# Performance work log

Hardware: AMD Instinct MI355X
Metric: run time of the kernel (lower is better)

## Reference

```python
import jax, jax.numpy as jnp
import numpy as np

N_QUBITS = 4
N_LAYERS = 2


def _ry(theta):
    # PennyLane RY(theta) = [[cos(t/2), -sin(t/2)], [sin(t/2), cos(t/2)]]
    c = jnp.cos(theta / 2)
    s = jnp.sin(theta / 2)
    return jnp.stack([jnp.stack([c, -s]), jnp.stack([s, c])]).astype(jnp.complex64)


def _rz(theta):
    # PennyLane RZ(theta) = diag(exp(-i t/2), exp(+i t/2))
    e = jnp.exp(-0.5j * theta.astype(jnp.complex64))
    return jnp.diag(jnp.stack([e, jnp.conj(e)]))


def _apply_1q(state, U, wire):
    # state: (2,)*N_QUBITS complex; contract U into axis `wire`
    state = jnp.tensordot(U, state, axes=((1,), (wire,)))
    return jnp.moveaxis(state, 0, wire)


def _cnot(state, ctrl, tgt):
    s = jnp.moveaxis(state, ctrl, 0)
    t2 = tgt - 1 if tgt > ctrl else tgt
    s1 = jnp.flip(s[1], axis=t2)  # X on target where control == 1
    return jnp.moveaxis(jnp.stack([s[0], s1]), 0, ctrl)


def _circuit(angles, weights):
    # angles: (N_QUBITS,), weights: (N_LAYERS, N_QUBITS, 2)
    state = jnp.zeros((2,) * N_QUBITS, jnp.complex64).at[(0,) * N_QUBITS].set(1.0)
    for i in range(N_QUBITS):
        state = _apply_1q(state, _ry(angles[i]), i)
    for l in range(N_LAYERS):
        for i in range(N_QUBITS):
            state = _apply_1q(state, _ry(weights[l, i, 0]), i)
            state = _apply_1q(state, _rz(weights[l, i, 1]), i)
        for i in range(N_QUBITS - 1):
            state = _cnot(state, i, i + 1)
        state = _cnot(state, N_QUBITS - 1, 0)
    probs = jnp.abs(state) ** 2
    p = probs.reshape(2, -1).sum(axis=1)  # marginal on wire 0
    return p[0] - p[1]  # <Z_0>


def setup_inputs() -> dict:
    key = jax.random.key(0)
    ks = jax.random.split(key, 6)
    B = 65536
    return {
        "x": jax.random.normal(ks[0], (B, 256), jnp.float32),
        "W1": jax.random.normal(ks[1], (64, 256), jnp.float32) * 0.0625,
        "b1": jax.random.normal(ks[2], (64,), jnp.float32) * 0.01,
        "W2": jax.random.normal(ks[3], (4, 64), jnp.float32) * 0.125,
        "b2": jax.random.normal(ks[4], (4,), jnp.float32) * 0.01,
        "q_weights": jax.random.normal(ks[5], (N_LAYERS, N_QUBITS, 2), jnp.float32) * 0.1,
    }


def reference(x, W1, b1, W2, b2, q_weights):
    h = jax.nn.relu(x @ W1.T + b1)          # [B, 64]
    angles = jnp.tanh(h @ W2.T + b2)         # [B, 4]
    z = jax.vmap(lambda a: _circuit(a, q_weights))(angles)  # [B]
    return z[:, None]                        # [B, 1]
```

## Files before the change

### kernel.cpp

```cpp
#include <hip/hip_runtime.h>
#include <math.h>

typedef _Float16 half8   __attribute__((ext_vector_type(8)));
typedef _Float16 half4v  __attribute__((ext_vector_type(4)));
typedef float    float4v __attribute__((ext_vector_type(4)));

#define BM    64
#define KDIM  256
#define HSW   65

__global__ void w1_cvt(const float* __restrict__ W1, _Float16* __restrict__ w1h)
{
    int i = (blockIdx.x * 256 + threadIdx.x) * 4;
    float4v v = *(const float4v*)(W1 + i);
    half4v h;
    h[0] = (_Float16)v[0]; h[1] = (_Float16)v[1];
    h[2] = (_Float16)v[2]; h[3] = (_Float16)v[3];
    *(half4v*)(w1h + i) = h;
}

__global__ __launch_bounds__(256, 4)
void qc_fused(const float* __restrict__ x,
              const _Float16* __restrict__ w1h,
              const float* __restrict__ b1,
              const float* __restrict__ W2,
              const float* __restrict__ b2,
              const float* __restrict__ qw,
              float* __restrict__ out)
{
    __shared__ float hs[BM * HSW];
    __shared__ float angs[BM * 4];
    __shared__ float trig[32];

    const int tid  = threadIdx.x;
    const int lane = tid & 63;
    const int wv   = tid >> 6;
    const int m    = lane & 15;
    const int q    = lane >> 4;
    const int row0 = blockIdx.x * BM;

    if (tid < 8) {
        int l = tid >> 2, i = tid & 3;
        float wy = qw[(l * 4 + i) * 2 + 0];
        float wz = qw[(l * 4 + i) * 2 + 1];
        float sy, cy, sz, cz;
        sincosf(0.5f * wy, &sy, &cy);
        sincosf(0.5f * wz, &sz, &cz);
        trig[(l * 4 + i) * 4 + 0] = cy;
        trig[(l * 4 + i) * 4 + 1] = sy;
        trig[(l * 4 + i) * 4 + 2] = cz;
        trig[(l * 4 + i) * 4 + 3] = sz;
    }

    const float* xrow = x + (size_t)(row0 + wv * 16 + m) * KDIM + q * 8;
    half8 afr[8];
    #pragma unroll
    for (int f = 0; f < 8; ++f) {
        float4v v0 = *(const float4v*)(xrow + f * 32);
        float4v v1 = *(const float4v*)(xrow + f * 32 + 4);
        afr[f][0] = (_Float16)v0[0]; afr[f][1] = (_Float16)v0[1];
        afr[f][2] = (_Float16)v0[2]; afr[f][3] = (_Float16)v0[3];
        afr[f][4] = (_Float16)v1[0]; afr[f][5] = (_Float16)v1[1];
        afr[f][6] = (_Float16)v1[2]; afr[f][7] = (_Float16)v1[3];
    }

    float b1v[4];
    #pragma unroll
    for (int b = 0; b < 4; ++b) b1v[b] = b1[16 * b + m];

    float4v acc[4] = {};
    #pragma unroll
    for (int f = 0; f < 8; ++f) {
        const int ko = f * 32 + q * 8;
        #pragma unroll
        for (int b = 0; b < 4; ++b) {
            half8 bf = *(const half8*)(w1h + (size_t)(16 * b + m) * KDIM + ko);
            acc[b] = __builtin_amdgcn_mfma_f32_16x16x32_f16(afr[f], bf, acc[b], 0, 0, 0);
        }
    }

    #pragma unroll
    for (int b = 0; b < 4; ++b) {
        #pragma unroll
        for (int i = 0; i < 4; ++i) {
            int row = wv * 16 + q * 4 + i;
            int col = 16 * b + m;
            hs[row * HSW + col] = fmaxf(acc[b][i] + b1v[b], 0.0f);
        }
    }
    __syncthreads();

    {
        int r = tid & 63, qi = tid >> 6;
        float s = b2[qi];
        #pragma unroll 8
        for (int k = 0; k < 64; ++k)
            s = fmaf(hs[r * HSW + k], W2[qi * 64 + k], s);
        angs[r * 4 + qi] = tanhf(s);
    }
    __syncthreads();

    if (tid < 64) {
        float ca[4], sa[4];
        #pragma unroll
        for (int i = 0; i < 4; ++i)
            __sincosf(0.5f * angs[tid * 4 + i], &sa[i], &ca[i]);

        float re[16], im[16];
        #pragma unroll
        for (int idx = 0; idx < 16; ++idx) {
            re[idx] = (idx & 8 ? sa[0] : ca[0]) * (idx & 4 ? sa[1] : ca[1]) *
                      (idx & 2 ? sa[2] : ca[2]) * (idx & 1 ? sa[3] : ca[3]);
            im[idx] = 0.0f;
        }
        #pragma unroll
        for (int l = 0; l < 2; ++l) {
            #pragma unroll
            for (int i = 0; i < 4; ++i) {
                const float cy = trig[(l * 4 + i) * 4 + 0];
                const float sy = trig[(l * 4 + i) * 4 + 1];
                const float cz = trig[(l * 4 + i) * 4 + 2];
                const float sz = trig[(l * 4 + i) * 4 + 3];
                const int mq = 8 >> i;
                #pragma unroll
                for (int idx = 0; idx < 16; ++idx) {
                    if (!(idx & mq)) {
                        int j = idx | mq;
                        float ar = re[idx], ai = im[idx], br = re[j], bi = im[j];
                        re[idx] = fmaf(cy, ar, -sy * br);
                        im[idx] = fmaf(cy, ai, -sy * bi);
                        re[j]   = fmaf(sy, ar,  cy * br);
                        im[j]   = fmaf(sy, ai,  cy * bi);
                    }
                }
                #pragma unroll
                for (int idx = 0; idx < 16; ++idx) {
                    float sgn = (idx & mq) ? sz : -sz;
                    float ar = re[idx], ai = im[idx];
                    re[idx] = fmaf(ar, cz, -ai * sgn);
                    im[idx] = fmaf(ar, sgn, ai * cz);
                }
            }
            #pragma unroll
            for (int c = 0; c < 4; ++c) {
                int t  = (c + 1) & 3;
                int mc = 8 >> c, mt = 8 >> t;
                #pragma unroll
                for (int idx = 0; idx < 16; ++idx) {
                    if ((idx & mc) && !(idx & mt)) {
                        int j = idx | mt;
                        float tr = re[idx]; re[idx] = re[j]; re[j] = tr;
                        float ti = im[idx]; im[idx] = im[j]; im[j] = ti;
                    }
                }
            }
        }
        float z = 0.0f;
        #pragma unroll
        for (int idx = 0; idx < 16; ++idx) {
            float p = re[idx] * re[idx] + im[idx] * im[idx];
            z += (idx & 8) ? -p : p;
        }
        out[row0 + tid] = z;
    }
}

extern "C" void kernel_launch(void* const* d_in, const int* in_sizes, int n_in,
                              void* d_out, int out_size, void* d_ws, size_t ws_size,
                              hipStream_t stream) {
    const float* x  = (const float*)d_in[0];
    const float* W1 = (const float*)d_in[1];
    const float* b1 = (const float*)d_in[2];
    const float* W2 = (const float*)d_in[3];
    const float* b2 = (const float*)d_in[4];
    const float* qw = (const float*)d_in[5];
    float* out = (float*)d_out;
    _Float16* w1h = (_Float16*)d_ws;

    w1_cvt<<<16, 256, 0, stream>>>(W1, w1h);
    const int B = in_sizes[0] / KDIM;
    qc_fused<<<B / BM, 256, 0, stream>>>(x, w1h, b1, W2, b2, qw, out);
}
```

Before: 117.9 us.

## Fuse W1 fp16 conversion into main kernel via padded LDS staging

Drops the separate W1 conversion kernel launch. Each block now converts W1 to fp16 and stages it in padded shared memory, which the MFMA B-operand loads then read instead of global memory. The x loads are split into two halves so the second half's global loads overlap the first MFMA pass, and the LDS buffer is reused for the hidden activations after a barrier. The cost is that every block redoes the W1 conversion and uses more LDS, which may lower occupancy.

```diff
diff --git a/kernel.cpp b/kernel.cpp
--- a/kernel.cpp
+++ b/kernel.cpp
@@ -7,30 +7,24 @@
 
 #define BM    64
 #define KDIM  256
+#define WSTR  264
 #define HSW   65
-
-__global__ void w1_cvt(const float* __restrict__ W1, _Float16* __restrict__ w1h)
-{
-    int i = (blockIdx.x * 256 + threadIdx.x) * 4;
-    float4v v = *(const float4v*)(W1 + i);
-    half4v h;
-    h[0] = (_Float16)v[0]; h[1] = (_Float16)v[1];
-    h[2] = (_Float16)v[2]; h[3] = (_Float16)v[3];
-    *(half4v*)(w1h + i) = h;
-}
 
 __global__ __launch_bounds__(256, 4)
 void qc_fused(const float* __restrict__ x,
-              const _Float16* __restrict__ w1h,
+              const float* __restrict__ W1,
               const float* __restrict__ b1,
               const float* __restrict__ W2,
               const float* __restrict__ b2,
               const float* __restrict__ qw,
               float* __restrict__ out)
 {
-    __shared__ float hs[BM * HSW];
+    __shared__ __align__(16) unsigned char smem_raw[64 * WSTR * 2];
     __shared__ float angs[BM * 4];
     __shared__ float trig[32];
+
+    _Float16* whs = (_Float16*)smem_raw;
+    float*    hs  = (float*)smem_raw;
 
     const int tid  = threadIdx.x;
     const int lane = tid & 63;
@@ -53,31 +47,76 @@
     }
 
     const float* xrow = x + (size_t)(row0 + wv * 16 + m) * KDIM + q * 8;
-    half8 afr[8];
-    #pragma unroll
-    for (int f = 0; f < 8; ++f) {
-        float4v v0 = *(const float4v*)(xrow + f * 32);
-        float4v v1 = *(const float4v*)(xrow + f * 32 + 4);
-        afr[f][0] = (_Float16)v0[0]; afr[f][1] = (_Float16)v0[1];
-        afr[f][2] = (_Float16)v0[2]; afr[f][3] = (_Float16)v0[3];
-        afr[f][4] = (_Float16)v1[0]; afr[f][5] = (_Float16)v1[1];
-        afr[f][6] = (_Float16)v1[2]; afr[f][7] = (_Float16)v1[3];
+
+    float4v xv[8];
+    #pragma unroll
+    for (int f = 0; f < 4; ++f) {
+        xv[2 * f]     = *(const float4v*)(xrow + f * 32);
+        xv[2 * f + 1] = *(const float4v*)(xrow + f * 32 + 4);
     }
 
     float b1v[4];
     #pragma unroll
     for (int b = 0; b < 4; ++b) b1v[b] = b1[16 * b + m];
 
+    {
+        const float* wsrc = W1 + tid * 4;
+        _Float16*    wdst = &whs[wv * WSTR + lane * 4];
+        #pragma unroll 4
+        for (int j = 0; j < 16; ++j) {
+            float4v v = *(const float4v*)(wsrc + j * 1024);
+            half4v h;
+            h[0] = (_Float16)v[0]; h[1] = (_Float16)v[1];
+            h[2] = (_Float16)v[2]; h[3] = (_Float16)v[3];
+            *(half4v*)(wdst + j * 4 * WSTR) = h;
+        }
+    }
+
+    half8 af[8];
+    #pragma unroll
+    for (int f = 0; f < 4; ++f) {
+        #pragma unroll
+        for (int j = 0; j < 4; ++j) {
+            af[f][j]     = (_Float16)xv[2 * f][j];
+            af[f][4 + j] = (_Float16)xv[2 * f + 1][j];
+        }
+    }
+    #pragma unroll
+    for (int f = 4; f < 8; ++f) {
+        xv[2 * (f - 4)]     = *(const float4v*)(xrow + f * 32);
+        xv[2 * (f - 4) + 1] = *(const float4v*)(xrow + f * 32 + 4);
+    }
+
+    __syncthreads();
+
     float4v acc[4] = {};
     #pragma unroll
-    for (int f = 0; f < 8; ++f) {
+    for (int f = 0; f < 4; ++f) {
         const int ko = f * 32 + q * 8;
         #pragma unroll
         for (int b = 0; b < 4; ++b) {
-            half8 bf = *(const half8*)(w1h + (size_t)(16 * b + m) * KDIM + ko);
-            acc[b] = __builtin_amdgcn_mfma_f32_16x16x32_f16(afr[f], bf, acc[b], 0, 0, 0);
-        }
-    }
+            half8 bf = *(const half8*)&whs[(16 * b + m) * WSTR + ko];
+            acc[b] = __builtin_amdgcn_mfma_f32_16x16x32_f16(af[f], bf, acc[b], 0, 0, 0);
+        }
+    }
+    #pragma unroll
+    for (int f = 4; f < 8; ++f) {
+        #pragma unroll
+        for (int j = 0; j < 4; ++j) {
+            af[f][j]     = (_Float16)xv[2 * (f - 4)][j];
+            af[f][4 + j] = (_Float16)xv[2 * (f - 4) + 1][j];
+        }
+    }
+    #pragma unroll
+    for (int f = 4; f < 8; ++f) {
+        const int ko = f * 32 + q * 8;
+        #pragma unroll
+        for (int b = 0; b < 4; ++b) {
+            half8 bf = *(const half8*)&whs[(16 * b + m) * WSTR + ko];
+            acc[b] = __builtin_amdgcn_mfma_f32_16x16x32_f16(af[f], bf, acc[b], 0, 0, 0);
+        }
+    }
+    __syncthreads();
 
     #pragma unroll
     for (int b = 0; b < 4; ++b) {
@@ -175,9 +214,6 @@
     const float* b2 = (const float*)d_in[4];
     const float* qw = (const float*)d_in[5];
     float* out = (float*)d_out;
-    _Float16* w1h = (_Float16*)d_ws;
-
-    w1_cvt<<<16, 256, 0, stream>>>(W1, w1h);
     const int B = in_sizes[0] / KDIM;
-    qc_fused<<<B / BM, 256, 0, stream>>>(x, w1h, b1, W2, b2, qw, out);
+    qc_fused<<<B / BM, 256, 0, stream>>>(x, W1, b1, W2, b2, qw, out);
 }
```

Result: faster. 105.1 us (-10.8%).

## Switch GEMM to 32x32x16 MFMA with 2x2 wave tiling and prefetched x chunks

Applied to the files above, without the earlier changes.

Each wave now computes a 32x32 output tile with the 32x32x16 MFMA instead of a 16x64 strip of 16x16x32 MFMAs. Each wave keeps its slice of W1 resident in registers and streams x in four chunks, so the loads for the next chunk are issued before the current chunk's MFMAs run. The aim is to cut redundant W1 loads per wave, use larger MFMAs and overlap global loads with compute. Each x row is now loaded by two waves instead of one, register pressure goes up, and the occupancy hint drops from 4 to 3 blocks per CU.

```diff
diff --git a/kernel.cpp b/kernel.cpp
--- a/kernel.cpp
+++ b/kernel.cpp
@@ -4,6 +4,7 @@
 typedef _Float16 half8   __attribute__((ext_vector_type(8)));
 typedef _Float16 half4v  __attribute__((ext_vector_type(4)));
 typedef float    float4v __attribute__((ext_vector_type(4)));
+typedef float    float16v __attribute__((ext_vector_type(16)));
 
 #define BM    64
 #define KDIM  256
@@ -19,7 +20,7 @@
     *(half4v*)(w1h + i) = h;
 }
 
-__global__ __launch_bounds__(256, 4)
+__global__ __launch_bounds__(256, 3)
 void qc_fused(const float* __restrict__ x,
               const _Float16* __restrict__ w1h,
               const float* __restrict__ b1,
@@ -35,8 +36,10 @@
     const int tid  = threadIdx.x;
     const int lane = tid & 63;
     const int wv   = tid >> 6;
-    const int m    = lane & 15;
-    const int q    = lane >> 4;
+    const int rg   = wv & 1;
+    const int cg   = wv >> 1;
+    const int n    = lane & 31;
+    const int hg   = lane >> 5;
     const int row0 = blockIdx.x * BM;
 
     if (tid < 8) {
@@ -52,40 +55,54 @@
         trig[(l * 4 + i) * 4 + 3] = sz;
     }
 
-    const float* xrow = x + (size_t)(row0 + wv * 16 + m) * KDIM + q * 8;
-    half8 afr[8];
+    const float* xrow = x + (size_t)(row0 + rg * 32 + n) * KDIM + hg * 8;
+    const _Float16* wrow = w1h + (size_t)(cg * 32 + n) * KDIM + hg * 8;
+
+    float4v xv[8];
     #pragma unroll
-    for (int f = 0; f < 8; ++f) {
-        float4v v0 = *(const float4v*)(xrow + f * 32);
-        float4v v1 = *(const float4v*)(xrow + f * 32 + 4);
-        afr[f][0] = (_Float16)v0[0]; afr[f][1] = (_Float16)v0[1];
-        afr[f][2] = (_Float16)v0[2]; afr[f][3] = (_Float16)v0[3];
-        afr[f][4] = (_Float16)v1[0]; afr[f][5] = (_Float16)v1[1];
-        afr[f][6] = (_Float16)v1[2]; afr[f][7] = (_Float16)v1[3];
-    }
-
-    float b1v[4];
+    for (int s = 0; s < 4; ++s) {
+        xv[2 * s]     = *(const float4v*)(xrow + s * 16);
+        xv[2 * s + 1] = *(const float4v*)(xrow + s * 16 + 4);
+    }
+
+    half8 wfr[16];
     #pragma unroll
-    for (int b = 0; b < 4; ++b) b1v[b] = b1[16 * b + m];
-
-    float4v acc[4] = {};
+    for (int s = 0; s < 16; ++s)
+        wfr[s] = *(const half8*)(wrow + s * 16);
+
+    const float b1c = b1[cg * 32 + n];
+
+    float16v acc = {};
+    half8 af[4];
     #pragma unroll
-    for (int f = 0; f < 8; ++f) {
-        const int ko = f * 32 + q * 8;
-        #pragma unroll
-        for (int b = 0; b < 4; ++b) {
-            half8 bf = *(const half8*)(w1h + (size_t)(16 * b + m) * KDIM + ko);
-            acc[b] = __builtin_amdgcn_mfma_f32_16x16x32_f16(afr[f], bf, acc[b], 0, 0, 0);
-        }
-    }
-
-    #pragma unroll
-    for (int b = 0; b < 4; ++b) {
-        #pragma unroll
-        for (int i = 0; i < 4; ++i) {
-            int row = wv * 16 + q * 4 + i;
-            int col = 16 * b + m;
-            hs[row * HSW + col] = fmaxf(acc[b][i] + b1v[b], 0.0f);
+    for (int c = 0; c < 4; ++c) {
+        #pragma unroll
+        for (int s = 0; s < 4; ++s) {
+            #pragma unroll
+            for (int j = 0; j < 4; ++j) {
+                af[s][j]     = (_Float16)xv[2 * s][j];
+                af[s][4 + j] = (_Float16)xv[2 * s + 1][j];
+            }
+        }
+        if (c < 3) {
+            const float* xc = xrow + (c + 1) * 64;
+            #pragma unroll
+            for (int s = 0; s < 4; ++s) {
+                xv[2 * s]     = *(const float4v*)(xc + s * 16);
+                xv[2 * s + 1] = *(const float4v*)(xc + s * 16 + 4);
+            }
+        }
+        #pragma unroll
+        for (int s = 0; s < 4; ++s)
+            acc = __builtin_amdgcn_mfma_f32_32x32x16_f16(af[s], wfr[c * 4 + s], acc, 0, 0, 0);
+    }
+
+    {
+        const int col = cg * 32 + n;
+        #pragma unroll
+        for (int reg = 0; reg < 16; ++reg) {
+            int row = rg * 32 + (reg & 3) + 8 * (reg >> 2) + 4 * hg;
+            hs[row * HSW + col] = fmaxf(acc[reg] + b1c, 0.0f);
         }
     }
     __syncthreads();
```

After: 123.4 us. 4.7% more time.
